# Kernel optimization log

Hardware: AMD Instinct MI355X
Metric: run time of the kernel (lower is better)

Reference implementation:

```python
import jax, jax.numpy as jnp
import numpy as np

NBINS = 256
NCH = 3


def _channel_hists(img):
    """img: [B, 3, H, W] float with values in [0, 256).
    Returns [3, 256] histogram counts, summed over the batch (matches
    cv2.calcHist per channel accumulated over images)."""
    idx = jnp.clip(img, 0.0, 255.0).astype(jnp.int32)          # bin = floor(v)
    offs = (jnp.arange(NCH, dtype=jnp.int32) * NBINS)[None, :, None, None]
    flat = (idx + offs).reshape(-1)                             # [B*3*H*W]
    h = jnp.zeros(NCH * NBINS, dtype=img.dtype).at[flat].add(1.0)
    return h.reshape(NCH, NBINS)


def _bhattacharyya_sum(h1, h2):
    """OpenCV HISTCMP_BHATTACHARYYA per channel, summed over channels.
    d = sqrt(1 - sum(sqrt(H1*H2)) / (N * sqrt(mean(H1)*mean(H2))))"""
    s = jnp.sum(jnp.sqrt(h1 * h2), axis=-1)                     # [3]
    denom = jnp.sqrt(h1.mean(-1) * h2.mean(-1)) * NBINS         # [3]
    d = jnp.sqrt(jnp.maximum(1.0 - s / denom, 0.0))
    return jnp.sum(d)


def setup_inputs() -> dict:
    key = jax.random.key(0)
    k1, k2 = jax.random.split(key)
    shape = (32, 3, 512, 512)
    # pixel values in [0, 256) like real image data
    inp = jax.random.uniform(k1, shape, dtype=jnp.float32) * 256.0
    lab = jax.random.uniform(k2, shape, dtype=jnp.float32) * 256.0
    return {"input": inp, "label": lab}


def reference(input, label):
    h_in = _channel_hists(input)    # [3, 256]
    h_lb = _channel_hists(label)    # [3, 256]
    return _bhattacharyya_sum(h_in, h_lb)
```

## Files before the change

### kernel.cpp

```cpp
#include <hip/hip_runtime.h>

#define NBINS 256
#define NCH 3
#define HW_LOG2 18
#define NHIST (2 * NCH * NBINS)

__global__ __launch_bounds__(256) void hist_kernel(
    const float* __restrict__ a, const float* __restrict__ b,
    unsigned int* __restrict__ gh, long long n4) {
    __shared__ unsigned int sh[NHIST];
    const int tid = threadIdx.x;
    for (int i = tid; i < NHIST; i += blockDim.x) sh[i] = 0u;
    __syncthreads();

    const float4* __restrict__ a4 = (const float4*)a;
    const float4* __restrict__ b4 = (const float4*)b;
    const long long stride = (long long)gridDim.x * blockDim.x;

    for (long long i = (long long)blockIdx.x * blockDim.x + tid; i < n4; i += stride) {
        const int ch = (int)((i >> (HW_LOG2 - 2)) % 3);
        unsigned int* __restrict__ ha = &sh[ch * NBINS];
        unsigned int* __restrict__ hb = &sh[(NCH + ch) * NBINS];

        const float4 va = a4[i];
        const float4 vb = b4[i];

        atomicAdd(&ha[(int)fminf(fmaxf(va.x, 0.f), 255.f)], 1u);
        atomicAdd(&ha[(int)fminf(fmaxf(va.y, 0.f), 255.f)], 1u);
        atomicAdd(&ha[(int)fminf(fmaxf(va.z, 0.f), 255.f)], 1u);
        atomicAdd(&ha[(int)fminf(fmaxf(va.w, 0.f), 255.f)], 1u);
        atomicAdd(&hb[(int)fminf(fmaxf(vb.x, 0.f), 255.f)], 1u);
        atomicAdd(&hb[(int)fminf(fmaxf(vb.y, 0.f), 255.f)], 1u);
        atomicAdd(&hb[(int)fminf(fmaxf(vb.z, 0.f), 255.f)], 1u);
        atomicAdd(&hb[(int)fminf(fmaxf(vb.w, 0.f), 255.f)], 1u);
    }
    __syncthreads();

    for (int i = tid; i < NHIST; i += blockDim.x) {
        const unsigned int v = sh[i];
        if (v) atomicAdd(&gh[i], v);
    }
}

__device__ __forceinline__ double block_reduce256(double v, double* sh4) {
    const int t = threadIdx.x;
    const int lane = t & 63, w = t >> 6;
    #pragma unroll
    for (int o = 32; o > 0; o >>= 1) v += __shfl_down(v, o, 64);
    if (lane == 0) sh4[w] = v;
    __syncthreads();
    double r = sh4[0] + sh4[1] + sh4[2] + sh4[3];
    __syncthreads();
    return r;
}

__global__ __launch_bounds__(256) void bhat_kernel(
    const unsigned int* __restrict__ gh, float* __restrict__ out) {
    __shared__ double sh4[4];
    const int t = threadIdx.x;
    double result = 0.0;
    #pragma unroll
    for (int ch = 0; ch < NCH; ++ch) {
        const double h1 = (double)gh[ch * NBINS + t];
        const double h2 = (double)gh[(NCH + ch) * NBINS + t];
        const double s  = block_reduce256(sqrt(h1 * h2), sh4);
        const double s1 = block_reduce256(h1, sh4);
        const double s2 = block_reduce256(h2, sh4);
        const double denom = sqrt((s1 / (double)NBINS) * (s2 / (double)NBINS)) * (double)NBINS;
        const double v = 1.0 - s / denom;
        result += sqrt(v > 0.0 ? v : 0.0);
    }
    if (t == 0) out[0] = (float)result;
}

extern "C" void kernel_launch(void* const* d_in, const int* in_sizes, int n_in,
                              void* d_out, int out_size, void* d_ws, size_t ws_size,
                              hipStream_t stream) {
    const float* input = (const float*)d_in[0];
    const float* label = (const float*)d_in[1];
    float* out = (float*)d_out;
    unsigned int* gh = (unsigned int*)d_ws;

    const long long n  = (long long)in_sizes[0];
    const long long n4 = n / 4;

    hipMemsetAsync(gh, 0, NHIST * sizeof(unsigned int), stream);

    const int block = 256;
    const int grid = 2048;
    hist_kernel<<<grid, block, 0, stream>>>(input, label, gh, n4);
    bhat_kernel<<<1, 256, 0, stream>>>(gh, out);
}
```

Baseline: 240.0 us.

## Replace shared-memory atomics with per-thread packed 8-bit private histograms

Each thread keeps a private histogram of byte-packed counters in LDS, updated with plain adds instead of atomics. Blocks are assigned to a single (array, channel) job, so the channel index is fixed per block. A final pass sums the packed bytes per bin before the global atomic add. This removes LDS atomic contention and serialization. The cost is 64KB of LDS per block, which lowers occupancy, and the 8-bit counters depend on the fixed image shape keeping per-thread counts under 256.

```diff
diff --git a/kernel.cpp b/kernel.cpp
--- a/kernel.cpp
+++ b/kernel.cpp
@@ -2,44 +2,77 @@
 
 #define NBINS 256
 #define NCH 3
-#define HW_LOG2 18
 #define NHIST (2 * NCH * NBINS)
+#define HW 262144
+#define HW4 65536
+#define BATCH 32
+#define JOB_N4 (BATCH * HW4)
+#define BLOCKS_PER_JOB 384
+#define THREADS 256
 
-__global__ __launch_bounds__(256) void hist_kernel(
+__device__ __forceinline__ void bump(unsigned int* lbase, float v) {
+    const int bin = (int)fminf(fmaxf(v, 0.f), 255.f);
+    unsigned int* p = lbase + (bin >> 2) * 64;
+    *p += 1u << ((bin & 3) << 3);
+}
+
+__global__ __launch_bounds__(THREADS) void hist_kernel(
     const float* __restrict__ a, const float* __restrict__ b,
-    unsigned int* __restrict__ gh, long long n4) {
-    __shared__ unsigned int sh[NHIST];
-    const int tid = threadIdx.x;
-    for (int i = tid; i < NHIST; i += blockDim.x) sh[i] = 0u;
+    unsigned int* __restrict__ gh) {
+    __shared__ unsigned int sh[16384];
+    const int tid  = threadIdx.x;
+    const int wave = tid >> 6;
+    const int lane = tid & 63;
+
+    uint4* shv = (uint4*)sh;
+    #pragma unroll
+    for (int i = 0; i < 16; ++i)
+        shv[tid + i * THREADS] = make_uint4(0u, 0u, 0u, 0u);
     __syncthreads();
 
-    const float4* __restrict__ a4 = (const float4*)a;
-    const float4* __restrict__ b4 = (const float4*)b;
-    const long long stride = (long long)gridDim.x * blockDim.x;
+    const int job        = blockIdx.x / BLOCKS_PER_JOB;
+    const int blockInJob = blockIdx.x % BLOCKS_PER_JOB;
+    const int arr = job / NCH;
+    const int ch  = job % NCH;
 
-    for (long long i = (long long)blockIdx.x * blockDim.x + tid; i < n4; i += stride) {
-        const int ch = (int)((i >> (HW_LOG2 - 2)) % 3);
-        unsigned int* __restrict__ ha = &sh[ch * NBINS];
-        unsigned int* __restrict__ hb = &sh[(NCH + ch) * NBINS];
+    const float4* __restrict__ src = (const float4*)(arr ? b : a);
+    unsigned int* const lbase = &sh[wave * 4096 + lane];
 
-        const float4 va = a4[i];
-        const float4 vb = b4[i];
-
-        atomicAdd(&ha[(int)fminf(fmaxf(va.x, 0.f), 255.f)], 1u);
-        atomicAdd(&ha[(int)fminf(fmaxf(va.y, 0.f), 255.f)], 1u);
-        atomicAdd(&ha[(int)fminf(fmaxf(va.z, 0.f), 255.f)], 1u);
-        atomicAdd(&ha[(int)fminf(fmaxf(va.w, 0.f), 255.f)], 1u);
-        atomicAdd(&hb[(int)fminf(fmaxf(vb.x, 0.f), 255.f)], 1u);
-        atomicAdd(&hb[(int)fminf(fmaxf(vb.y, 0.f), 255.f)], 1u);
-        atomicAdd(&hb[(int)fminf(fmaxf(vb.z, 0.f), 255.f)], 1u);
-        atomicAdd(&hb[(int)fminf(fmaxf(vb.w, 0.f), 255.f)], 1u);
+    const unsigned stride = BLOCKS_PER_JOB * THREADS;
+    for (unsigned i = blockInJob * THREADS + tid; i < JOB_N4; i += 2 * stride) {
+        const unsigned j = i + stride;
+        const unsigned gi = ((i >> 16) * NCH + ch) * HW4 + (i & (HW4 - 1));
+        const float4 va = src[gi];
+        const bool pb = (j < JOB_N4);
+        float4 vb;
+        if (pb) {
+            const unsigned gj = ((j >> 16) * NCH + ch) * HW4 + (j & (HW4 - 1));
+            vb = src[gj];
+        }
+        bump(lbase, va.x); bump(lbase, va.y);
+        bump(lbase, va.z); bump(lbase, va.w);
+        if (pb) {
+            bump(lbase, vb.x); bump(lbase, vb.y);
+            bump(lbase, vb.z); bump(lbase, vb.w);
+        }
     }
     __syncthreads();
 
-    for (int i = tid; i < NHIST; i += blockDim.x) {
-        const unsigned int v = sh[i];
-        if (v) atomicAdd(&gh[i], v);
+    unsigned int sum = 0;
+    const int grp = tid >> 2;
+    const int sh8 = (tid & 3) << 3;
+    #pragma unroll
+    for (int w = 0; w < 4; ++w) {
+        const unsigned int* base = &sh[w * 4096 + grp * 64];
+        #pragma unroll
+        for (int c = 0; c < 16; ++c) {
+            const int cc = (c + tid) & 15;
+            const uint4 q = *(const uint4*)(base + cc * 4);
+            sum += ((q.x >> sh8) & 0xFFu) + ((q.y >> sh8) & 0xFFu)
+                 + ((q.z >> sh8) & 0xFFu) + ((q.w >> sh8) & 0xFFu);
+        }
     }
+    atomicAdd(&gh[(arr * NCH + ch) * NBINS + tid], sum);
 }
 
 __device__ __forceinline__ double block_reduce256(double v, double* sh4) {
@@ -81,13 +114,8 @@
     float* out = (float*)d_out;
     unsigned int* gh = (unsigned int*)d_ws;
 
-    const long long n  = (long long)in_sizes[0];
-    const long long n4 = n / 4;
-
     hipMemsetAsync(gh, 0, NHIST * sizeof(unsigned int), stream);
 
-    const int block = 256;
-    const int grid = 2048;
-    hist_kernel<<<grid, block, 0, stream>>>(input, label, gh, n4);
+    hist_kernel<<<6 * BLOCKS_PER_JOB, THREADS, 0, stream>>>(input, label, gh);
     bhat_kernel<<<1, 256, 0, stream>>>(gh, out);
 }
```

After: 237.2 us. Within noise of the previous version (-1.1%).
